# Kernel optimization log

Measured on AMD Instinct MI355X. Metric: run time of the kernel, lower is better.

## Reference

```python
import jax, jax.numpy as jnp
import numpy as np

B, N, CIN, COUT, K, E = 2048, 64, 128, 256, 3, 256
EPS = 1e-5


def setup_inputs() -> dict:
    key = jax.random.key(0)
    ks = jax.random.split(key, 8)
    x = jax.random.normal(ks[0], (B, N, CIN), dtype=jnp.float32)
    edge_index = jax.random.randint(ks[1], (2, E), 0, N, dtype=jnp.int32)
    W = jax.random.normal(ks[2], (CIN, COUT), dtype=jnp.float32) / np.sqrt(CIN)
    b_gcn = jnp.zeros((COUT,), jnp.float32)
    w_conv = jax.random.normal(ks[3], (COUT, COUT, K), dtype=jnp.float32) / np.sqrt(COUT * K)
    b_conv = jnp.zeros((COUT,), jnp.float32)
    gamma = jnp.ones((COUT,), jnp.float32)
    beta = jnp.zeros((COUT,), jnp.float32)
    return {"x": x, "W": W, "b_gcn": b_gcn, "w_conv": w_conv, "b_conv": b_conv,
            "gamma": gamma, "beta": beta, "edge_index": edge_index}


def reference(x, W, b_gcn, w_conv, b_conv, gamma, beta, edge_index):
    Bq, Nn, _ = x.shape
    Co = W.shape[1]
    # ---- GCNConv (PyG semantics: xW, add self-loops, symmetric norm, + bias) ----
    src, dst = edge_index[0], edge_index[1]
    loop = jnp.arange(Nn, dtype=edge_index.dtype)
    src2 = jnp.concatenate([src, loop])           # [E+N]
    dst2 = jnp.concatenate([dst, loop])
    deg = jnp.zeros((Nn,), x.dtype).at[dst2].add(1.0)
    dinv = jnp.where(deg > 0, jax.lax.rsqrt(deg), 0.0)
    norm = dinv[src2] * dinv[dst2]                # [E+N]
    xw = jnp.einsum('bnc,co->bno', x, W)          # [B, N, Co]
    msgs = xw[:, src2, :] * norm[None, :, None]   # [B, E+N, Co]
    x_gcn = jnp.zeros((Bq, Nn, Co), x.dtype).at[:, dst2, :].add(msgs) + b_gcn
    # ---- temporal Conv1d over batch_seq axis, shared weights across nodes ----
    xt = x_gcn.transpose(1, 2, 0)                 # [N, Co, B]  (time = batch_seq)
    pad = K // 2
    y = jax.lax.conv_general_dilated(xt, w_conv, (1,), [(pad, pad)],
                                     dimension_numbers=('NCH', 'OIH', 'NCH'))
    y = y + b_conv[None, :, None]                 # [N, Co, B]
    # ---- BatchNorm1d (training-mode batch stats) + ReLU ----
    y = y.transpose(2, 1, 0)                      # [B, Co, N]
    mean = y.mean(axis=(0, 2), keepdims=True)
    var = ((y - mean) ** 2).mean(axis=(0, 2), keepdims=True)
    y = (y - mean) * jax.lax.rsqrt(var + EPS)
    y = gamma[None, :, None] * y + beta[None, :, None]
    y = jax.nn.relu(y)
    # dropout is identity in eval mode
    return y.transpose(0, 2, 1)                   # [B, N, Co]
```

## Files before the change

### kernel.cpp

```cpp
#include <hip/hip_runtime.h>
#include <hip/hip_bf16.h>

typedef __attribute__((ext_vector_type(8))) unsigned short us8;
typedef __attribute__((ext_vector_type(4))) unsigned short us4;
typedef __attribute__((ext_vector_type(8))) short short8;
typedef __attribute__((ext_vector_type(4))) float f32x4;

#define BB 2048
#define NN 64
#define CIN 128
#define CO 256
#define KWIN 3
#define EE 256
#define NE 320
#define EPSBN 1e-5f

static __device__ __forceinline__ void gload_lds16(const unsigned short* g, unsigned short* l) {
    __builtin_amdgcn_global_load_lds(
        (const __attribute__((address_space(1))) unsigned int*)g,
        (__attribute__((address_space(3))) unsigned int*)l,
        16, 0, 0);
}

static __device__ __forceinline__ float bf2f(unsigned short u) {
    return __uint_as_float(((unsigned int)u) << 16);
}

static __device__ __forceinline__ unsigned short f2bfu(float f) {
    unsigned int u = __float_as_uint(f);
    u = (u + 0x7FFFu + ((u >> 16) & 1u)) >> 16;
    return (unsigned short)u;
}

__global__ __launch_bounds__(320) void k_setup(const int* __restrict__ ei,
                                               __hip_bfloat16* __restrict__ Ahat) {
    __shared__ int s_cnt[NN * NN];
    __shared__ int s_deg[NN];
    __shared__ float s_dinv[NN];
    const int t = threadIdx.x;
    for (int i = t; i < NN * NN; i += 320) s_cnt[i] = 0;
    if (t < NN) s_deg[t] = 0;
    __syncthreads();
    int src, dst;
    if (t < EE) { src = ei[t]; dst = ei[EE + t]; }
    else        { src = t - EE; dst = t - EE; }
    atomicAdd(&s_deg[dst], 1);
    atomicAdd(&s_cnt[dst * NN + src], 1);
    __syncthreads();
    if (t < NN) s_dinv[t] = rsqrtf((float)s_deg[t]);
    __syncthreads();
    for (int i = t; i < NN * NN; i += 320) {
        const int n = i >> 6, m = i & 63;
        Ahat[i] = __float2bfloat16((float)s_cnt[i] * s_dinv[m] * s_dinv[n]);
    }
}

__global__ __launch_bounds__(256) void k_weights(const float* __restrict__ W,
                                                 const float* __restrict__ wconv,
                                                 __hip_bfloat16* __restrict__ Wt,
                                                 __hip_bfloat16* __restrict__ W2t) {
    const int idx = blockIdx.x * 256 + threadIdx.x;
    if (idx < CO * CIN) {
        const int o = idx >> 7, c = idx & 127;
        Wt[idx] = __float2bfloat16(W[c * CO + o]);
    }
    const int j = idx - CO * CIN;
    if (j >= 0 && j < CO * KWIN * CO) {
        const int o = j / 768, q = j - o * 768;
        const int kk = q >> 8, i = q & 255;
        W2t[j] = __float2bfloat16(wconv[(o * CO + i) * KWIN + kk]);
    }
}

__global__ __launch_bounds__(256) void k_gcn(const float* __restrict__ x,
                                             const __hip_bfloat16* __restrict__ Ahat_,
                                             const __hip_bfloat16* __restrict__ Wt_,
                                             const float* __restrict__ bgcn,
                                             __hip_bfloat16* __restrict__ xgcn_) {
    __shared__ __align__(16) unsigned short sx[64 * 128];
    __shared__ __align__(16) unsigned short stm[256 * 64];
    const unsigned short* Ahat = (const unsigned short*)Ahat_;
    const unsigned short* Wt   = (const unsigned short*)Wt_;
    unsigned short* xgcn = (unsigned short*)xgcn_;

    const int b = blockIdx.x, tid = threadIdx.x;
    const int lane = tid & 63, wid = tid >> 6;
    const int llo = lane & 15, lhi = lane >> 4;

#pragma unroll
    for (int r = 0; r < 4; ++r) {
        const int f = tid + 256 * r;
        const int m = f >> 4, c0 = (f & 15) * 8;
        const float4* src = (const float4*)(x + ((size_t)b * NN + m) * CIN + c0);
        const float4 v0 = src[0], v1 = src[1];
        unsigned short t8[8] = {f2bfu(v0.x), f2bfu(v0.y), f2bfu(v0.z), f2bfu(v0.w),
                                f2bfu(v1.x), f2bfu(v1.y), f2bfu(v1.z), f2bfu(v1.w)};
        *(us8*)&sx[m * 128 + (c0 ^ ((m & 7) << 3))] = *(const us8*)t8;
    }
    __syncthreads();

    f32x4 acc1[4][4];
#pragma unroll
    for (int p = 0; p < 4; ++p)
#pragma unroll
        for (int q = 0; q < 4; ++q) acc1[p][q] = (f32x4){0.f, 0.f, 0.f, 0.f};
#pragma unroll
    for (int s = 0; s < 4; ++s) {
        const int k0 = s * 32 + lhi * 8;
        short8 af[4], bf[4];
#pragma unroll
        for (int p = 0; p < 4; ++p) {
            const int m = p * 16 + llo;
            af[p] = *(const short8*)&sx[m * 128 + (k0 ^ ((m & 7) << 3))];
        }
#pragma unroll
        for (int q = 0; q < 4; ++q) {
            const int o = wid * 64 + q * 16 + llo;
            bf[q] = *(const short8*)&Wt[o * 128 + k0];
        }
#pragma unroll
        for (int p = 0; p < 4; ++p)
#pragma unroll
            for (int q = 0; q < 4; ++q)
                acc1[p][q] = __builtin_amdgcn_mfma_f32_16x16x32_bf16(af[p], bf[q], acc1[p][q], 0, 0, 0);
    }
#pragma unroll
    for (int p = 0; p < 4; ++p)
#pragma unroll
        for (int q = 0; q < 4; ++q) {
            const int o = wid * 64 + q * 16 + llo;
            const int bm = p * 16 + lhi * 4;
            unsigned short t4[4] = {f2bfu(acc1[p][q][0]), f2bfu(acc1[p][q][1]),
                                    f2bfu(acc1[p][q][2]), f2bfu(acc1[p][q][3])};
            *(us4*)&stm[o * 64 + (bm ^ ((o & 7) << 3))] = *(const us4*)t4;
        }

    f32x4 acc2[4][4];
#pragma unroll
    for (int p = 0; p < 4; ++p)
#pragma unroll
        for (int q = 0; q < 4; ++q) acc2[p][q] = (f32x4){0.f, 0.f, 0.f, 0.f};
#pragma unroll
    for (int s = 0; s < 2; ++s) {
        const int k0 = s * 32 + lhi * 8;
        short8 af[4], bf[4];
#pragma unroll
        for (int p = 0; p < 4; ++p) {
            const int n = p * 16 + llo;
            af[p] = *(const short8*)&Ahat[n * 64 + k0];
        }
#pragma unroll
        for (int q = 0; q < 4; ++q) {
            const int o = wid * 64 + q * 16 + llo;
            bf[q] = *(const short8*)&stm[o * 64 + (k0 ^ ((o & 7) << 3))];
        }
#pragma unroll
        for (int p = 0; p < 4; ++p)
#pragma unroll
            for (int q = 0; q < 4; ++q)
                acc2[p][q] = __builtin_amdgcn_mfma_f32_16x16x32_bf16(af[p], bf[q], acc2[p][q], 0, 0, 0);
    }

    float bg[4];
#pragma unroll
    for (int q = 0; q < 4; ++q) bg[q] = bgcn[wid * 64 + q * 16 + llo];
    unsigned short* dst = xgcn + (size_t)b * NN * CO;
#pragma unroll
    for (int p = 0; p < 4; ++p)
#pragma unroll
        for (int q = 0; q < 4; ++q) {
            const int o = wid * 64 + q * 16 + llo;
#pragma unroll
            for (int reg = 0; reg < 4; ++reg) {
                const int n = p * 16 + lhi * 4 + reg;
                dst[n * CO + o] = f2bfu(acc2[p][q][reg] + bg[q]);
            }
        }
}

__global__ __launch_bounds__(256) void k_conv(const __hip_bfloat16* __restrict__ xgcn_,
                                              const __hip_bfloat16* __restrict__ W2t_,
                                              const float* __restrict__ bconv,
                                              __hip_bfloat16* __restrict__ y_,
                                              float* __restrict__ partials) {
    __shared__ __align__(16) unsigned short sA[136 * 64];
    __shared__ __align__(16) unsigned short sB[2][128 * 64];
    const unsigned short* xgcn = (const unsigned short*)xgcn_;
    const unsigned short* W2t  = (const unsigned short*)W2t_;
    unsigned short* y = (unsigned short*)y_;

    const int tt = blockIdx.x, ot = blockIdx.y, n = blockIdx.z;
    const int tid = threadIdx.x;
    const int lane = tid & 63, wid = tid >> 6;
    const int t0 = tt * 128, o0 = ot * 128;
    const int wm0 = (wid >> 1) * 64, wn0 = (wid & 1) * 64;
    const int lhi = lane >> 4, llo = lane & 15;

    f32x4 acc[4][4];
#pragma unroll
    for (int m = 0; m < 4; ++m)
#pragma unroll
        for (int nn = 0; nn < 4; ++nn) acc[m][nn] = (f32x4){0.f, 0.f, 0.f, 0.f};

    const int srsub = lane >> 3;
    const int scol  = (((lane & 7) ^ srsub) << 3);

    for (int g = 0; g < 4; ++g) {
        const int i0 = g * 64;
        for (int iss = wid; iss < 17; iss += 4) {
            const int rbase = iss * 8;
            int tg = t0 - 1 + rbase + srsub;
            tg = min(max(tg, 0), BB - 1);
            gload_lds16(xgcn + ((size_t)tg * NN + n) * CO + i0 + scol, sA + rbase * 64);
        }
#pragma unroll
        for (int iss = 0; iss < 4; ++iss) {
            const int rbase = wid * 32 + iss * 8;
            gload_lds16(W2t + (size_t)(o0 + rbase + srsub) * (CO * KWIN) + i0 + scol,
                        sB[0] + rbase * 64);
        }
        __syncthreads();
        if (tt == 0 || tt == 15) {
            const int zr = (tt == 0) ? 0 : 129;
            if (tid < 8) *(uint4*)&sA[zr * 64 + tid * 8] = make_uint4(0u, 0u, 0u, 0u);
            __syncthreads();
        }
#pragma unroll
        for (int kk = 0; kk < 3; ++kk) {
            if (kk < 2) {
                const int q0 = (kk + 1) * 256 + i0;
#pragma unroll
                for (int iss = 0; iss < 4; ++iss) {
                    const int rbase = wid * 32 + iss * 8;
                    gload_lds16(W2t + (size_t)(o0 + rbase + srsub) * (CO * KWIN) + q0 + scol,
                                sB[(kk + 1) & 1] + rbase * 64);
                }
            }
#pragma unroll
            for (int s = 0; s < 2; ++s) {
                const int cu = s * 32 + lhi * 8;
                short8 af[4], bf[4];
#pragma unroll
                for (int m = 0; m < 4; ++m) {
                    const int sr = wm0 + m * 16 + llo + kk;
                    af[m] = *(const short8*)&sA[sr * 64 + (cu ^ ((sr & 7) << 3))];
                }
#pragma unroll
                for (int nn = 0; nn < 4; ++nn) {
                    const int row = wn0 + nn * 16 + llo;
                    bf[nn] = *(const short8*)&sB[kk & 1][row * 64 + (cu ^ ((row & 7) << 3))];
                }
#pragma unroll
                for (int m = 0; m < 4; ++m)
#pragma unroll
                    for (int nn = 0; nn < 4; ++nn)
                        acc[m][nn] = __builtin_amdgcn_mfma_f32_16x16x32_bf16(af[m], bf[nn], acc[m][nn], 0, 0, 0);
            }
            __syncthreads();
        }
    }

    float bc[4], s1v[4], s2v[4];
#pragma unroll
    for (int nn = 0; nn < 4; ++nn) {
        bc[nn] = bconv[o0 + wn0 + nn * 16 + llo];
        s1v[nn] = 0.f; s2v[nn] = 0.f;
    }
#pragma unroll
    for (int m = 0; m < 4; ++m) {
#pragma unroll
        for (int reg = 0; reg < 4; ++reg) {
            const int trow = t0 + wm0 + m * 16 + lhi * 4 + reg;
            unsigned short* dst = y + ((size_t)trow * NN + n) * CO + o0 + wn0 + llo;
#pragma unroll
            for (int nn = 0; nn < 4; ++nn) {
                const float v = acc[m][nn][reg] + bc[nn];
                dst[nn * 16] = f2bfu(v);
                s1v[nn] += v;
                s2v[nn] += v * v;
            }
        }
    }
    float* sred1 = (float*)sA;
    float* sred2 = sred1 + 1024;
    const int rg = (wid >> 1) * 4 + lhi;
#pragma unroll
    for (int nn = 0; nn < 4; ++nn) {
        const int cl = wn0 + nn * 16 + llo;
        sred1[rg * 128 + cl] = s1v[nn];
        sred2[rg * 128 + cl] = s2v[nn];
    }
    __syncthreads();
    if (tid < 128) {
        float a = 0.f, b2 = 0.f;
#pragma unroll
        for (int r = 0; r < 8; ++r) { a += sred1[r * 128 + tid]; b2 += sred2[r * 128 + tid]; }
        float* pb = partials + (size_t)((n * 2 + ot) * 16 + tt) * 256;
        pb[tid * 2]     = a;
        pb[tid * 2 + 1] = b2;
    }
}

__global__ __launch_bounds__(256) void k_bnstats(const float* __restrict__ partials,
                                                 const float* __restrict__ gamma,
                                                 const float* __restrict__ beta,
                                                 float* __restrict__ scl,
                                                 float* __restrict__ shf) {
    const int o = blockIdx.x, tid = threadIdx.x;
    const int ot = o >> 7, c = o & 127;
    float s1 = 0.f, s2 = 0.f;
    for (int i = tid; i < 1024; i += 256) {
        const int nn = i >> 4, tt = i & 15;
        const float* p = partials + ((size_t)((nn * 2 + ot) * 16 + tt)) * 256 + c * 2;
        s1 += p[0]; s2 += p[1];
    }
    __shared__ float r1[256], r2[256];
    r1[tid] = s1; r2[tid] = s2;
    __syncthreads();
    for (int s = 128; s > 0; s >>= 1) {
        if (tid < s) { r1[tid] += r1[tid + s]; r2[tid] += r2[tid + s]; }
        __syncthreads();
    }
    if (tid == 0) {
        const float inv = 1.f / (float)((size_t)BB * NN);
        const float mean = r1[0] * inv;
        const float var  = r2[0] * inv - mean * mean;
        const float sc = gamma[o] * rsqrtf(var + EPSBN);
        scl[o] = sc;
        shf[o] = beta[o] - mean * sc;
    }
}

__global__ __launch_bounds__(256) void k_apply(const unsigned short* __restrict__ y,
                                               float* __restrict__ out,
                                               const float* __restrict__ scl,
                                               const float* __restrict__ shf) {
    __shared__ float ssc[CO], ssh[CO];
    const int tid = threadIdx.x;
    ssc[tid] = scl[tid]; ssh[tid] = shf[tid];
    __syncthreads();
    const size_t total8 = (size_t)BB * NN * CO / 8;
    float4* out4 = (float4*)out;
    for (size_t i = (size_t)blockIdx.x * 256 + tid; i < total8; i += (size_t)gridDim.x * 256) {
        const us8 v = *(const us8*)(y + i * 8);
        const int ob = (int)((i * 8) & (CO - 1));
        float4 r0, r1;
        r0.x = fmaxf(0.f, bf2f(v[0]) * ssc[ob + 0] + ssh[ob + 0]);
        r0.y = fmaxf(0.f, bf2f(v[1]) * ssc[ob + 1] + ssh[ob + 1]);
        r0.z = fmaxf(0.f, bf2f(v[2]) * ssc[ob + 2] + ssh[ob + 2]);
        r0.w = fmaxf(0.f, bf2f(v[3]) * ssc[ob + 3] + ssh[ob + 3]);
        r1.x = fmaxf(0.f, bf2f(v[4]) * ssc[ob + 4] + ssh[ob + 4]);
        r1.y = fmaxf(0.f, bf2f(v[5]) * ssc[ob + 5] + ssh[ob + 5]);
        r1.z = fmaxf(0.f, bf2f(v[6]) * ssc[ob + 6] + ssh[ob + 6]);
        r1.w = fmaxf(0.f, bf2f(v[7]) * ssc[ob + 7] + ssh[ob + 7]);
        out4[i * 2]     = r0;
        out4[i * 2 + 1] = r1;
    }
}

extern "C" void kernel_launch(void* const* d_in, const int* in_sizes, int n_in,
                              void* d_out, int out_size, void* d_ws, size_t ws_size,
                              hipStream_t stream) {
    const float* x     = (const float*)d_in[0];
    const float* W     = (const float*)d_in[1];
    const float* bgcn  = (const float*)d_in[2];
    const float* wconv = (const float*)d_in[3];
    const float* bconv = (const float*)d_in[4];
    const float* gamma = (const float*)d_in[5];
    const float* beta  = (const float*)d_in[6];
    const int*   ei    = (const int*)d_in[7];
    float* out = (float*)d_out;

    char* ws = (char*)d_ws;
    size_t off = 0;
    __hip_bfloat16* xgcn = (__hip_bfloat16*)(ws + off); off += (size_t)BB * NN * CO * 2;
    __hip_bfloat16* ybuf = (__hip_bfloat16*)(ws + off); off += (size_t)BB * NN * CO * 2;
    __hip_bfloat16* W2t  = (__hip_bfloat16*)(ws + off); off += (size_t)CO * KWIN * CO * 2;
    __hip_bfloat16* Ahat = (__hip_bfloat16*)(ws + off); off += (size_t)NN * NN * 2;
    __hip_bfloat16* Wt   = (__hip_bfloat16*)(ws + off); off += (size_t)CO * CIN * 2;
    float* partials = (float*)(ws + off); off += (size_t)2048 * 256 * 4;
    float* scl = (float*)(ws + off); off += 256 * 4;
    float* shf = (float*)(ws + off); off += 256 * 4;

    k_setup<<<1, 320, 0, stream>>>(ei, Ahat);
    k_weights<<<896, 256, 0, stream>>>(W, wconv, Wt, W2t);
    k_gcn<<<BB, 256, 0, stream>>>(x, Ahat, Wt, bgcn, xgcn);
    k_conv<<<dim3(16, 2, 64), 256, 0, stream>>>(xgcn, W2t, bconv, ybuf, partials);
    k_bnstats<<<256, 256, 0, stream>>>(partials, gamma, beta, scl, shf);
    k_apply<<<2048, 256, 0, stream>>>((const unsigned short*)ybuf, out, scl, shf);
}
```

Measured before the change: 156.2 us.

## Store GCN output node-major and stage full time tile in LDS for conv

```diff
diff --git a/kernel.cpp b/kernel.cpp
--- a/kernel.cpp
+++ b/kernel.cpp
@@ -164,7 +164,6 @@
     float bg[4];
 #pragma unroll
     for (int q = 0; q < 4; ++q) bg[q] = bgcn[wid * 64 + q * 16 + llo];
-    unsigned short* dst = xgcn + (size_t)b * NN * CO;
 #pragma unroll
     for (int p = 0; p < 4; ++p)
 #pragma unroll
@@ -173,7 +172,7 @@
 #pragma unroll
             for (int reg = 0; reg < 4; ++reg) {
                 const int n = p * 16 + lhi * 4 + reg;
-                dst[n * CO + o] = f2bfu(acc2[p][q][reg] + bg[q]);
+                xgcn[((size_t)n * BB + b) * CO + o] = f2bfu(acc2[p][q][reg] + bg[q]);
             }
         }
 }
@@ -183,8 +182,7 @@
                                               const float* __restrict__ bconv,
                                               __hip_bfloat16* __restrict__ y_,
                                               float* __restrict__ partials) {
-    __shared__ __align__(16) unsigned short sA[136 * 64];
-    __shared__ __align__(16) unsigned short sB[2][128 * 64];
+    __shared__ __align__(16) unsigned short sA[130 * 256];
     const unsigned short* xgcn = (const unsigned short*)xgcn_;
     const unsigned short* W2t  = (const unsigned short*)W2t_;
     unsigned short* y = (unsigned short*)y_;
@@ -202,62 +200,44 @@
 #pragma unroll
         for (int nn = 0; nn < 4; ++nn) acc[m][nn] = (f32x4){0.f, 0.f, 0.f, 0.f};
 
-    const int srsub = lane >> 3;
-    const int scol  = (((lane & 7) ^ srsub) << 3);
-
-    for (int g = 0; g < 4; ++g) {
-        const int i0 = g * 64;
-        for (int iss = wid; iss < 17; iss += 4) {
-            const int rbase = iss * 8;
-            int tg = t0 - 1 + rbase + srsub;
-            tg = min(max(tg, 0), BB - 1);
-            gload_lds16(xgcn + ((size_t)tg * NN + n) * CO + i0 + scol, sA + rbase * 64);
-        }
-#pragma unroll
-        for (int iss = 0; iss < 4; ++iss) {
-            const int rbase = wid * 32 + iss * 8;
-            gload_lds16(W2t + (size_t)(o0 + rbase + srsub) * (CO * KWIN) + i0 + scol,
-                        sB[0] + rbase * 64);
-        }
+    {
+        const int rsub = lane >> 5;
+        const int g = lane & 31;
+        for (int iss = wid; iss < 65; iss += 4) {
+            const int r = 2 * iss + rsub;
+            int bg = t0 - 1 + r;
+            bg = min(max(bg, 0), BB - 1);
+            const int col = ((g ^ (r & 7)) << 3);
+            gload_lds16(xgcn + ((size_t)n * BB + bg) * CO + col, sA + iss * 512);
+        }
+    }
+    __syncthreads();
+    if (tt == 0 || tt == 15) {
+        const int zr = (tt == 0) ? 0 : 129;
+        if (tid < 32) *(uint4*)&sA[zr * 256 + tid * 8] = make_uint4(0u, 0u, 0u, 0u);
         __syncthreads();
-        if (tt == 0 || tt == 15) {
-            const int zr = (tt == 0) ? 0 : 129;
-            if (tid < 8) *(uint4*)&sA[zr * 64 + tid * 8] = make_uint4(0u, 0u, 0u, 0u);
-            __syncthreads();
-        }
-#pragma unroll
-        for (int kk = 0; kk < 3; ++kk) {
-            if (kk < 2) {
-                const int q0 = (kk + 1) * 256 + i0;
-#pragma unroll
-                for (int iss = 0; iss < 4; ++iss) {
-                    const int rbase = wid * 32 + iss * 8;
-                    gload_lds16(W2t + (size_t)(o0 + rbase + srsub) * (CO * KWIN) + q0 + scol,
-                                sB[(kk + 1) & 1] + rbase * 64);
-                }
-            }
-#pragma unroll
-            for (int s = 0; s < 2; ++s) {
-                const int cu = s * 32 + lhi * 8;
-                short8 af[4], bf[4];
-#pragma unroll
-                for (int m = 0; m < 4; ++m) {
-                    const int sr = wm0 + m * 16 + llo + kk;
-                    af[m] = *(const short8*)&sA[sr * 64 + (cu ^ ((sr & 7) << 3))];
-                }
-#pragma unroll
-                for (int nn = 0; nn < 4; ++nn) {
-                    const int row = wn0 + nn * 16 + llo;
-                    bf[nn] = *(const short8*)&sB[kk & 1][row * 64 + (cu ^ ((row & 7) << 3))];
-                }
-#pragma unroll
-                for (int m = 0; m < 4; ++m)
-#pragma unroll
-                    for (int nn = 0; nn < 4; ++nn)
-                        acc[m][nn] = __builtin_amdgcn_mfma_f32_16x16x32_bf16(af[m], bf[nn], acc[m][nn], 0, 0, 0);
-            }
-            __syncthreads();
-        }
+    }
+
+#pragma unroll 8
+    for (int kc = 0; kc < 24; ++kc) {
+        const int kk = kc >> 3;
+        const int G = (kc & 7) * 4 + lhi;
+        short8 af[4], bf[4];
+#pragma unroll
+        for (int m = 0; m < 4; ++m) {
+            const int sr = wm0 + m * 16 + llo + kk;
+            af[m] = *(const short8*)&sA[sr * 256 + ((G ^ (sr & 7)) << 3)];
+        }
+#pragma unroll
+        for (int q = 0; q < 4; ++q) {
+            const int o = o0 + wn0 + q * 16 + llo;
+            bf[q] = *(const short8*)&W2t[o * 768 + kk * 256 + (kc & 7) * 32 + lhi * 8];
+        }
+#pragma unroll
+        for (int m = 0; m < 4; ++m)
+#pragma unroll
+            for (int q = 0; q < 4; ++q)
+                acc[m][q] = __builtin_amdgcn_mfma_f32_16x16x32_bf16(af[m], bf[q], acc[m][q], 0, 0, 0);
     }
 
     float bc[4], s1v[4], s2v[4];
@@ -281,6 +261,7 @@
             }
         }
     }
+    __syncthreads();
     float* sred1 = (float*)sA;
     float* sred2 = sred1 + 1024;
     const int rg = (wid >> 1) * 4 + lhi;
```

Measured after the change: 209.3 us. 1.34x slower.
